# Performance work log

Hardware: AMD Instinct MI355X
Metric: run time of the kernel (lower is better)

The kernel has to match this reference:

```python
import jax, jax.numpy as jnp
import numpy as np

N_NODES = 100000
N_EDGES = 1600000
F_IN = 64
F_OUT = 64


def setup_inputs() -> dict:
    key = jax.random.key(0)
    k1, k2, k3 = jax.random.split(key, 3)
    x = jax.random.normal(k1, (1, 1, N_NODES, F_IN), dtype=jnp.float32)
    edge_index = jax.random.randint(k2, (2, N_EDGES), 0, N_NODES, dtype=jnp.int32)
    # xavier-init linear weight [F_IN, F_OUT], zero bias (xavier_zero_bias)
    scale = jnp.sqrt(2.0 / (F_IN + F_OUT)).astype(jnp.float32)
    weight = jax.random.normal(k3, (F_IN, F_OUT), dtype=jnp.float32) * scale
    bias = jnp.zeros((F_OUT,), dtype=jnp.float32)
    return {"x": x, "edge_index": edge_index, "weight": weight, "bias": bias}


def reference(x, edge_index, weight, bias):
    # x: [B, T, N, F_in]
    B, T, N, _ = x.shape
    # linear transform
    h = jnp.einsum('btnf,fo->btno', x, weight) + bias  # [B,T,N,F_out]
    # add self loops
    loops = jnp.arange(N, dtype=edge_index.dtype)
    src = jnp.concatenate([edge_index[0], loops])  # [E+N]
    dst = jnp.concatenate([edge_index[1], loops])  # [E+N]
    w = jnp.ones(src.shape[0], dtype=h.dtype)
    # symmetric GCN normalization: D^{-1/2} A D^{-1/2} (degree over dst)
    deg = jnp.zeros((N,), dtype=h.dtype).at[dst].add(w)
    inv_sqrt = jnp.clip(deg, 1e-9) ** -0.5
    norm = inv_sqrt[dst] * w * inv_sqrt[src]  # [E+N]
    # gather src features, scale by norm, scatter-add to dst
    msg = h[:, :, src, :] * norm[None, None, :, None]  # [B,T,E+N,F_out]
    out = jnp.zeros_like(h).at[:, :, dst, :].add(msg)  # [B,T,N,F_out]
    # GraphConvBase post: activation (gelu), dropout=0, norm=identity
    return jax.nn.gelu(out)
```

## Files before the change

### kernel.cpp

```cpp
#include <hip/hip_runtime.h>
#include <hip/hip_fp16.h>
#include <math.h>

#define N_NODES 100000
#define N_EDGES 1600000
#define F_DIM 64
#define BSH 9
#define BNODES 512
#define NBUCK ((N_NODES + BNODES - 1) / BNODES)
#define CAP 16384
#define EPT 32
#define TILE (256 * EPT)

__global__ __launch_bounds__(256) void init_k(int* __restrict__ bcur) {
    int i = blockIdx.x * 256 + threadIdx.x;
    if (i < NBUCK) bcur[i] = i * CAP;
}

__global__ __launch_bounds__(256) void pass1_k(const int* __restrict__ src,
                                               const int* __restrict__ dst,
                                               int* __restrict__ bcur,
                                               unsigned int* __restrict__ tmp, int E) {
    __shared__ int lcnt[NBUCK];
    __shared__ int lbase[NBUCK];
    for (int i = threadIdx.x; i < NBUCK; i += 256) lcnt[i] = 0;
    __syncthreads();

    int4 sreg[EPT / 4], dreg[EPT / 4];
    int base4 = blockIdx.x * (TILE / 4);
#pragma unroll
    for (int j = 0; j < EPT / 4; ++j) {
        int i4 = base4 + j * 256 + threadIdx.x;
        if (i4 < E / 4) {
            sreg[j] = ((const int4*)src)[i4];
            dreg[j] = ((const int4*)dst)[i4];
            atomicAdd(&lcnt[dreg[j].x >> BSH], 1);
            atomicAdd(&lcnt[dreg[j].y >> BSH], 1);
            atomicAdd(&lcnt[dreg[j].z >> BSH], 1);
            atomicAdd(&lcnt[dreg[j].w >> BSH], 1);
        } else {
            dreg[j].x = -1;
        }
    }
    __syncthreads();
    for (int b = threadIdx.x; b < NBUCK; b += 256) {
        int c = lcnt[b];
        lbase[b] = c ? atomicAdd(&bcur[b], c) : 0;
        lcnt[b] = 0;
    }
    __syncthreads();
#pragma unroll
    for (int j = 0; j < EPT / 4; ++j) {
        if (dreg[j].x >= 0) {
            int d, s, b, r;
            d = dreg[j].x; s = sreg[j].x; b = d >> BSH;
            r = atomicAdd(&lcnt[b], 1);
            tmp[lbase[b] + r] = (unsigned int)s | ((unsigned int)(d & (BNODES - 1)) << 17);
            d = dreg[j].y; s = sreg[j].y; b = d >> BSH;
            r = atomicAdd(&lcnt[b], 1);
            tmp[lbase[b] + r] = (unsigned int)s | ((unsigned int)(d & (BNODES - 1)) << 17);
            d = dreg[j].z; s = sreg[j].z; b = d >> BSH;
            r = atomicAdd(&lcnt[b], 1);
            tmp[lbase[b] + r] = (unsigned int)s | ((unsigned int)(d & (BNODES - 1)) << 17);
            d = dreg[j].w; s = sreg[j].w; b = d >> BSH;
            r = atomicAdd(&lcnt[b], 1);
            tmp[lbase[b] + r] = (unsigned int)s | ((unsigned int)(d & (BNODES - 1)) << 17);
        }
    }
}

__global__ __launch_bounds__(256) void passB_k(unsigned int* __restrict__ tmp,
                                               const int* __restrict__ bcur,
                                               unsigned int* __restrict__ rowinfo,
                                               float* __restrict__ inv) {
    __shared__ unsigned int buf[CAP];
    __shared__ int cnt[BNODES];
    __shared__ int cur[BNODES];
    __shared__ int ls[256];
    int b = blockIdx.x;
    int beg0 = b * CAP;
    int cntb = bcur[b] - beg0;

    cnt[threadIdx.x] = 0;
    cnt[threadIdx.x + 256] = 0;
    __syncthreads();
    for (int i = threadIdx.x; i < cntb; i += 256) {
        unsigned int v = tmp[beg0 + i];
        buf[i] = v;
        atomicAdd(&cnt[v >> 17], 1);
    }
    __syncthreads();

    int a0 = cnt[2 * threadIdx.x];
    int a1 = cnt[2 * threadIdx.x + 1];
    int tsum = a0 + a1;
    ls[threadIdx.x] = tsum;
    __syncthreads();
    for (int off = 1; off < 256; off <<= 1) {
        int p = (threadIdx.x >= off) ? ls[threadIdx.x - off] : 0;
        __syncthreads();
        ls[threadIdx.x] += p;
        __syncthreads();
    }
    int excl = ls[threadIdx.x] - tsum;
    int p0 = beg0 + excl;
    int p1 = p0 + a0;
    cur[2 * threadIdx.x] = p0;
    cur[2 * threadIdx.x + 1] = p1;
    int n0 = (b << BSH) + 2 * threadIdx.x;
    if (n0 < N_NODES) {
        rowinfo[n0] = (unsigned int)p0 | ((unsigned int)a0 << 22);
        inv[n0] = rsqrtf((float)(a0 + 1));
    }
    if (n0 + 1 < N_NODES) {
        rowinfo[n0 + 1] = (unsigned int)p1 | ((unsigned int)a1 << 22);
        inv[n0 + 1] = rsqrtf((float)(a1 + 1));
    }
    __syncthreads();

    for (int i = threadIdx.x; i < cntb; i += 256) {
        unsigned int v = buf[i];
        int pos = atomicAdd(&cur[v >> 17], 1);
        tmp[pos] = v & 0x1FFFFu;
    }
}

__global__ __launch_bounds__(256) void linear_k(const float* __restrict__ x,
                                                const float* __restrict__ W,
                                                const float* __restrict__ bias,
                                                const float* __restrict__ inv,
                                                __half* __restrict__ h, int N) {
    __shared__ float Ws[F_DIM][F_DIM];
    __shared__ float bs[F_DIM];
    for (int i = threadIdx.x; i < F_DIM * F_DIM; i += 256) Ws[i >> 6][i & 63] = W[i];
    if (threadIdx.x < F_DIM) bs[threadIdx.x] = bias[threadIdx.x];
    __syncthreads();

    int n = blockIdx.x * 256 + threadIdx.x;
    if (n >= N) return;

    float xr[F_DIM];
    const float4* xp = (const float4*)(x + (size_t)n * F_DIM);
#pragma unroll
    for (int k4 = 0; k4 < 16; ++k4) {
        float4 v = xp[k4];
        xr[k4 * 4 + 0] = v.x; xr[k4 * 4 + 1] = v.y;
        xr[k4 * 4 + 2] = v.z; xr[k4 * 4 + 3] = v.w;
    }
    float invn = inv[n];
    __half* hp = h + (size_t)n * F_DIM;
#pragma unroll 1
    for (int f0 = 0; f0 < F_DIM; f0 += 4) {
        float a0 = bs[f0 + 0], a1 = bs[f0 + 1], a2 = bs[f0 + 2], a3 = bs[f0 + 3];
#pragma unroll
        for (int k = 0; k < F_DIM; ++k) {
            float xv = xr[k];
            a0 += xv * Ws[k][f0 + 0];
            a1 += xv * Ws[k][f0 + 1];
            a2 += xv * Ws[k][f0 + 2];
            a3 += xv * Ws[k][f0 + 3];
        }
        union { __half2 h2[2]; float2 f2; } u;
        u.h2[0] = __floats2half2_rn(a0 * invn, a1 * invn);
        u.h2[1] = __floats2half2_rn(a2 * invn, a3 * invn);
        *((float2*)(hp + f0)) = u.f2;
    }
}

__device__ __forceinline__ float gelu1(float x) {
    float x3 = x * x * x;
    float t = tanhf(0.7978845608028654f * (x + 0.044715f * x3));
    return 0.5f * x * (1.0f + t);
}

__global__ __launch_bounds__(256) void gather_k(const __half* __restrict__ h,
                                                const float* __restrict__ inv,
                                                const unsigned int* __restrict__ rowinfo,
                                                const unsigned int* __restrict__ esrc,
                                                float* __restrict__ out, int N) {
    int n = blockIdx.x * 4 + (threadIdx.x >> 6);
    if (n >= N) return;
    int lane = threadIdx.x & 63;
    int eslot = lane >> 4;
    int fq = lane & 15;

    unsigned int ri = rowinfo[n];
    int beg = (int)(ri & 0x3FFFFFu);
    int deg = (int)(ri >> 22);

    float ax = 0.f, ay = 0.f, az = 0.f, aw = 0.f;
    int k = eslot;
    for (; k + 12 < deg; k += 16) {
        int s0 = (int)esrc[beg + k];
        int s1 = (int)esrc[beg + k + 4];
        int s2 = (int)esrc[beg + k + 8];
        int s3 = (int)esrc[beg + k + 12];
        float2 p0 = *((const float2*)(h + (size_t)s0 * F_DIM) + fq);
        float2 p1 = *((const float2*)(h + (size_t)s1 * F_DIM) + fq);
        float2 p2 = *((const float2*)(h + (size_t)s2 * F_DIM) + fq);
        float2 p3 = *((const float2*)(h + (size_t)s3 * F_DIM) + fq);
        union { float2 f; __half2 h2[2]; } u0, u1, u2, u3;
        u0.f = p0; u1.f = p1; u2.f = p2; u3.f = p3;
        float2 a, b;
        a = __half22float2(u0.h2[0]); b = __half22float2(u0.h2[1]);
        ax += a.x; ay += a.y; az += b.x; aw += b.y;
        a = __half22float2(u1.h2[0]); b = __half22float2(u1.h2[1]);
        ax += a.x; ay += a.y; az += b.x; aw += b.y;
        a = __half22float2(u2.h2[0]); b = __half22float2(u2.h2[1]);
        ax += a.x; ay += a.y; az += b.x; aw += b.y;
        a = __half22float2(u3.h2[0]); b = __half22float2(u3.h2[1]);
        ax += a.x; ay += a.y; az += b.x; aw += b.y;
    }
    for (; k < deg; k += 4) {
        int s0 = (int)esrc[beg + k];
        float2 p0 = *((const float2*)(h + (size_t)s0 * F_DIM) + fq);
        union { float2 f; __half2 h2[2]; } u0;
        u0.f = p0;
        float2 a = __half22float2(u0.h2[0]);
        float2 b = __half22float2(u0.h2[1]);
        ax += a.x; ay += a.y; az += b.x; aw += b.y;
    }
    ax += __shfl_xor(ax, 16); ay += __shfl_xor(ay, 16);
    az += __shfl_xor(az, 16); aw += __shfl_xor(aw, 16);
    ax += __shfl_xor(ax, 32); ay += __shfl_xor(ay, 32);
    az += __shfl_xor(az, 32); aw += __shfl_xor(aw, 32);

    if (eslot == 0) {
        float invn = inv[n];
        union { float2 f; __half2 h2[2]; } us;
        us.f = *((const float2*)(h + (size_t)n * F_DIM) + fq);
        float2 s0 = __half22float2(us.h2[0]);
        float2 s1 = __half22float2(us.h2[1]);
        float4 o;
        o.x = gelu1((ax + s0.x) * invn);
        o.y = gelu1((ay + s0.y) * invn);
        o.z = gelu1((az + s1.x) * invn);
        o.w = gelu1((aw + s1.y) * invn);
        ((float4*)(out + (size_t)n * F_DIM))[fq] = o;
    }
}

extern "C" void kernel_launch(void* const* d_in, const int* in_sizes, int n_in,
                              void* d_out, int out_size, void* d_ws, size_t ws_size,
                              hipStream_t stream) {
    const float* x    = (const float*)d_in[0];
    const int*   ei   = (const int*)d_in[1];
    const float* W    = (const float*)d_in[2];
    const float* bias = (const float*)d_in[3];
    float* out = (float*)d_out;

    const int* src = ei;
    const int* dst = ei + N_EDGES;

    unsigned int* tmp     = (unsigned int*)d_ws;
    unsigned int* rowinfo = tmp + (size_t)NBUCK * CAP;
    float*        inv     = (float*)(rowinfo + N_NODES);
    int*          bcur    = (int*)(inv + N_NODES);
    size_t off = (size_t)(bcur + NBUCK) - (size_t)d_ws;
    off = (off + 31) & ~(size_t)31;
    __half* h = (__half*)((char*)d_ws + off);

    init_k<<<(NBUCK + 255) / 256, 256, 0, stream>>>(bcur);
    pass1_k<<<(N_EDGES + TILE - 1) / TILE, 256, 0, stream>>>(src, dst, bcur, tmp, N_EDGES);
    passB_k<<<NBUCK, 256, 0, stream>>>(tmp, bcur, rowinfo, inv);
    linear_k<<<(N_NODES + 255) / 256, 256, 0, stream>>>(x, W, bias, inv, h, N_NODES);
    gather_k<<<(N_NODES + 3) / 4, 256, 0, stream>>>(h, inv, rowinfo, tmp, out, N_NODES);
}
```

Measured before the change: 125.0 us.

## Accumulate gather in half2, retune pass1 tile, passB and linear block sizes

The gather kernel now sums neighbour features with packed half2 adds and converts to float only after the loop. The aim is to remove the per-element half-to-float conversions and cut ALU work. Separately, pass1 processes fewer edges per thread (more blocks), passB uses 512 threads with one node per thread in the scan, and linear_k uses 128-thread blocks. Half-precision accumulation over many neighbours loses accuracy and could overflow, so the results may drift from the reference.

```diff
diff --git a/kernel.cpp b/kernel.cpp
--- a/kernel.cpp
+++ b/kernel.cpp
@@ -9,7 +9,7 @@
 #define BNODES 512
 #define NBUCK ((N_NODES + BNODES - 1) / BNODES)
 #define CAP 16384
-#define EPT 32
+#define EPT 8
 #define TILE (256 * EPT)
 
 __global__ __launch_bounds__(256) void init_k(int* __restrict__ bcur) {
@@ -69,74 +69,65 @@
     }
 }
 
-__global__ __launch_bounds__(256) void passB_k(unsigned int* __restrict__ tmp,
+__global__ __launch_bounds__(512) void passB_k(unsigned int* __restrict__ tmp,
                                                const int* __restrict__ bcur,
                                                unsigned int* __restrict__ rowinfo,
                                                float* __restrict__ inv) {
     __shared__ unsigned int buf[CAP];
     __shared__ int cnt[BNODES];
     __shared__ int cur[BNODES];
-    __shared__ int ls[256];
+    __shared__ int ls[BNODES];
     int b = blockIdx.x;
     int beg0 = b * CAP;
     int cntb = bcur[b] - beg0;
-
-    cnt[threadIdx.x] = 0;
-    cnt[threadIdx.x + 256] = 0;
-    __syncthreads();
-    for (int i = threadIdx.x; i < cntb; i += 256) {
+    int tid = threadIdx.x;
+
+    cnt[tid] = 0;
+    __syncthreads();
+    for (int i = tid; i < cntb; i += 512) {
         unsigned int v = tmp[beg0 + i];
         buf[i] = v;
         atomicAdd(&cnt[v >> 17], 1);
     }
     __syncthreads();
 
-    int a0 = cnt[2 * threadIdx.x];
-    int a1 = cnt[2 * threadIdx.x + 1];
-    int tsum = a0 + a1;
-    ls[threadIdx.x] = tsum;
-    __syncthreads();
-    for (int off = 1; off < 256; off <<= 1) {
-        int p = (threadIdx.x >= off) ? ls[threadIdx.x - off] : 0;
+    int a = cnt[tid];
+    ls[tid] = a;
+    __syncthreads();
+    for (int off = 1; off < BNODES; off <<= 1) {
+        int p = (tid >= off) ? ls[tid - off] : 0;
         __syncthreads();
-        ls[threadIdx.x] += p;
+        ls[tid] += p;
         __syncthreads();
     }
-    int excl = ls[threadIdx.x] - tsum;
-    int p0 = beg0 + excl;
-    int p1 = p0 + a0;
-    cur[2 * threadIdx.x] = p0;
-    cur[2 * threadIdx.x + 1] = p1;
-    int n0 = (b << BSH) + 2 * threadIdx.x;
-    if (n0 < N_NODES) {
-        rowinfo[n0] = (unsigned int)p0 | ((unsigned int)a0 << 22);
-        inv[n0] = rsqrtf((float)(a0 + 1));
-    }
-    if (n0 + 1 < N_NODES) {
-        rowinfo[n0 + 1] = (unsigned int)p1 | ((unsigned int)a1 << 22);
-        inv[n0 + 1] = rsqrtf((float)(a1 + 1));
-    }
-    __syncthreads();
-
-    for (int i = threadIdx.x; i < cntb; i += 256) {
+    int p0 = beg0 + ls[tid] - a;
+    cur[tid] = p0;
+    int n = (b << BSH) + tid;
+    if (n < N_NODES) {
+        rowinfo[n] = (unsigned int)p0 | ((unsigned int)a << 22);
+        inv[n] = rsqrtf((float)(a + 1));
+    }
+    __syncthreads();
+
+    for (int i = tid; i < cntb; i += 512) {
         unsigned int v = buf[i];
         int pos = atomicAdd(&cur[v >> 17], 1);
         tmp[pos] = v & 0x1FFFFu;
     }
 }
 
-__global__ __launch_bounds__(256) void linear_k(const float* __restrict__ x,
+__global__ __launch_bounds__(128) void linear_k(const float* __restrict__ x,
                                                 const float* __restrict__ W,
                                                 const float* __restrict__ bias,
                                                 const float* __restrict__ inv,
                                                 __half* __restrict__ h, int N) {
     __shared__ float Ws[F_DIM][F_DIM];
     __shared__ float bs[F_DIM];
-    for (int i = threadIdx.x; i < F_DIM * F_DIM; i += 256) Ws[i >> 6][i & 63] = W[i];
+    for (int i = threadIdx.x; i < F_DIM * F_DIM; i += 128) Ws[i >> 6][i & 63] = W[i];
     if (threadIdx.x < F_DIM) bs[threadIdx.x] = bias[threadIdx.x];
     __syncthreads();
 
-    int n = blockIdx.x * 256 + threadIdx.x;
+    int n = blockIdx.x * 128 + threadIdx.x;
     if (n >= N) return;
 
     float xr[F_DIM];
@@ -188,38 +179,32 @@
     int beg = (int)(ri & 0x3FFFFFu);
     int deg = (int)(ri >> 22);
 
-    float ax = 0.f, ay = 0.f, az = 0.f, aw = 0.f;
+    __half2 acc0 = __floats2half2_rn(0.f, 0.f);
+    __half2 acc1 = acc0;
     int k = eslot;
     for (; k + 12 < deg; k += 16) {
         int s0 = (int)esrc[beg + k];
         int s1 = (int)esrc[beg + k + 4];
         int s2 = (int)esrc[beg + k + 8];
         int s3 = (int)esrc[beg + k + 12];
-        float2 p0 = *((const float2*)(h + (size_t)s0 * F_DIM) + fq);
-        float2 p1 = *((const float2*)(h + (size_t)s1 * F_DIM) + fq);
-        float2 p2 = *((const float2*)(h + (size_t)s2 * F_DIM) + fq);
-        float2 p3 = *((const float2*)(h + (size_t)s3 * F_DIM) + fq);
         union { float2 f; __half2 h2[2]; } u0, u1, u2, u3;
-        u0.f = p0; u1.f = p1; u2.f = p2; u3.f = p3;
-        float2 a, b;
-        a = __half22float2(u0.h2[0]); b = __half22float2(u0.h2[1]);
-        ax += a.x; ay += a.y; az += b.x; aw += b.y;
-        a = __half22float2(u1.h2[0]); b = __half22float2(u1.h2[1]);
-        ax += a.x; ay += a.y; az += b.x; aw += b.y;
-        a = __half22float2(u2.h2[0]); b = __half22float2(u2.h2[1]);
-        ax += a.x; ay += a.y; az += b.x; aw += b.y;
-        a = __half22float2(u3.h2[0]); b = __half22float2(u3.h2[1]);
-        ax += a.x; ay += a.y; az += b.x; aw += b.y;
+        u0.f = *((const float2*)(h + (size_t)s0 * F_DIM) + fq);
+        u1.f = *((const float2*)(h + (size_t)s1 * F_DIM) + fq);
+        u2.f = *((const float2*)(h + (size_t)s2 * F_DIM) + fq);
+        u3.f = *((const float2*)(h + (size_t)s3 * F_DIM) + fq);
+        acc0 = __hadd2(acc0, __hadd2(__hadd2(u0.h2[0], u1.h2[0]), __hadd2(u2.h2[0], u3.h2[0])));
+        acc1 = __hadd2(acc1, __hadd2(__hadd2(u0.h2[1], u1.h2[1]), __hadd2(u2.h2[1], u3.h2[1])));
     }
     for (; k < deg; k += 4) {
         int s0 = (int)esrc[beg + k];
-        float2 p0 = *((const float2*)(h + (size_t)s0 * F_DIM) + fq);
         union { float2 f; __half2 h2[2]; } u0;
-        u0.f = p0;
-        float2 a = __half22float2(u0.h2[0]);
-        float2 b = __half22float2(u0.h2[1]);
-        ax += a.x; ay += a.y; az += b.x; aw += b.y;
-    }
+        u0.f = *((const float2*)(h + (size_t)s0 * F_DIM) + fq);
+        acc0 = __hadd2(acc0, u0.h2[0]);
+        acc1 = __hadd2(acc1, u0.h2[1]);
+    }
+    float2 a = __half22float2(acc0);
+    float2 b2 = __half22float2(acc1);
+    float ax = a.x, ay = a.y, az = b2.x, aw = b2.y;
     ax += __shfl_xor(ax, 16); ay += __shfl_xor(ay, 16);
     az += __shfl_xor(az, 16); aw += __shfl_xor(aw, 16);
     ax += __shfl_xor(ax, 32); ay += __shfl_xor(ay, 32);
@@ -262,7 +247,7 @@
 
     init_k<<<(NBUCK + 255) / 256, 256, 0, stream>>>(bcur);
     pass1_k<<<(N_EDGES + TILE - 1) / TILE, 256, 0, stream>>>(src, dst, bcur, tmp, N_EDGES);
-    passB_k<<<NBUCK, 256, 0, stream>>>(tmp, bcur, rowinfo, inv);
-    linear_k<<<(N_NODES + 255) / 256, 256, 0, stream>>>(x, W, bias, inv, h, N_NODES);
+    passB_k<<<NBUCK, 512, 0, stream>>>(tmp, bcur, rowinfo, inv);
+    linear_k<<<(N_NODES + 127) / 128, 128, 0, stream>>>(x, W, bias, inv, h, N_NODES);
     gather_k<<<(N_NODES + 3) / 4, 256, 0, stream>>>(h, inv, rowinfo, tmp, out, N_NODES);
 }
```

Result: slower. 131.1 us (+4.9%).
